# Performance work log

Hardware: AMD Instinct MI355X
Metric: run time of the kernel (lower is better)

Reference implementation:

```python
import jax, jax.numpy as jnp
import numpy as np

N, D, E, T, R, KMEM, DE = 50000, 128, 800000, 400000, 1, 32, 16
EPS = 1e-5
BETA_MAX = 5.0
GRAD_CLIP = 1.0
STATE_CLIP = 10.0
STEP = 0.1
DAMP = 0.9999  # update_damping=1.0 clamped to 1-1e-4 as in __init__


def segment_logsumexp(s, idx, n):
    # numerically-stable per-segment logsumexp; empty segments contribute 0
    m = jax.ops.segment_max(s, idx, num_segments=n)
    ms = jnp.where(jnp.isfinite(m), m, 0.0)
    z = jax.ops.segment_sum(jnp.exp(s - ms[idx]), idx, num_segments=n)
    return jnp.where(z > 0, jnp.log(jnp.maximum(z, 1e-30)) + ms, 0.0)


def setup_inputs() -> dict:
    key = jax.random.key(0)
    ks = jax.random.split(key, 24)
    inv1 = jnp.log(jnp.expm1(jnp.float32(1.0)))  # _inv_softplus(1.0)
    xav = 0.5 * np.sqrt(2.0 / (2 * D))  # xavier_uniform gain=0.5 ~ std
    inp = {
        'X': jax.random.normal(ks[0], (N, D), jnp.float32),
        'edge_attr': jax.random.normal(ks[1], (E, DE), jnp.float32),
        'ln_gamma': jnp.ones((D,), jnp.float32),
        'ln_beta': jnp.zeros((D,), jnp.float32),
        'W_Q2': jax.random.normal(ks[2], (D, D), jnp.float32) * xav,
        'W_K2': jax.random.normal(ks[3], (D, D), jnp.float32) * xav,
        'W_Q3': jax.random.normal(ks[4], (D, R * D), jnp.float32) * xav,
        'W_K3': jax.random.normal(ks[5], (D, R * D), jnp.float32) * xav,
        'T_tau': jax.random.normal(ks[6], (2, R, D), jnp.float32) * 0.02,
        'W_Qm': jax.random.normal(ks[7], (D, D), jnp.float32) * xav,
        'W_Km': jax.random.normal(ks[8], (D, D), jnp.float32) * xav,
        'B_mem': jax.random.normal(ks[9], (KMEM, D), jnp.float32) / np.sqrt(D),
        'We1': jax.random.normal(ks[10], (DE, D), jnp.float32) / np.sqrt(DE),
        'be1': jnp.zeros((D,), jnp.float32),
        'We2': jax.random.normal(ks[11], (D, 1), jnp.float32) / np.sqrt(D),
        'be2': jnp.zeros((1,), jnp.float32),
        'lambda_2': inv1, 'lambda_3': inv1, 'lambda_m': inv1,
        'beta_2': inv1, 'beta_3': inv1, 'beta_m': inv1,
        'c_2': jax.random.randint(ks[12], (E,), 0, N),
        'u_2': jax.random.randint(ks[13], (E,), 0, N),
        'c_3': jax.random.randint(ks[14], (T,), 0, N),
        'u_3': jax.random.randint(ks[15], (T,), 0, N),
        'v_3': jax.random.randint(ks[16], (T,), 0, N),
        't_tau': jax.random.randint(ks[17], (T,), 0, 2),
    }
    return inp


def reference(X, edge_attr, ln_gamma, ln_beta, W_Q2, W_K2, W_Q3, W_K3, T_tau,
              W_Qm, W_Km, B_mem, We1, be1, We2, be2,
              lambda_2, lambda_3, lambda_m, beta_2, beta_3, beta_m,
              c_2, u_2, c_3, u_3, v_3, t_tau):
    sqrt_d = jnp.sqrt(jnp.float32(D))

    def energy(Xv):
        mu = jnp.mean(Xv, axis=-1, keepdims=True)
        var = jnp.var(Xv, axis=-1, keepdims=True)
        G = (Xv - mu) * jax.lax.rsqrt(var + EPS) * ln_gamma + ln_beta
        # pairwise (order-2) energy over edge list
        b2 = jnp.minimum(jax.nn.softplus(beta_2), BETA_MAX)
        Q2, K2 = G @ W_Q2, G @ W_K2
        a2 = (jax.nn.gelu(edge_attr @ We1 + be1) @ We2 + be2)[:, 0]  # edge_mlp bias
        s2 = b2 * (jnp.sum(Q2[c_2] * K2[u_2], axis=-1) / sqrt_d) + a2  # [E]
        E2 = -(jax.nn.softplus(lambda_2) / b2) * jnp.sum(segment_logsumexp(s2, c_2, N))
        # triplet (order-3) energy with per-type tensor T_tau
        b3 = jnp.minimum(jax.nn.softplus(beta_3), BETA_MAX)
        Q3 = (G @ W_Q3).reshape(-1, R, D)
        K3 = (G @ W_K3).reshape(-1, R, D)
        s3 = b3 * jnp.einsum('erd,erd,erd,erd->e', Q3[c_3], K3[u_3], K3[v_3],
                             T_tau[t_tau]) / jnp.float32(D)  # [T]
        E3 = -(jax.nn.softplus(lambda_3) / b3) * jnp.sum(segment_logsumexp(s3, c_3, N))
        # memory-bank energy
        bm = jnp.minimum(jax.nn.softplus(beta_m), BETA_MAX)
        sm = bm * ((G @ W_Qm) @ (B_mem @ W_Km).T) / sqrt_d  # [N,K]
        Em = -(jax.nn.softplus(lambda_m) / bm) * jnp.sum(jax.nn.logsumexp(sm, axis=1))
        return E2 + E3 + Em

    Eval, gX = jax.value_and_grad(energy)(X)
    gn = jnp.maximum(jnp.linalg.norm(gX, axis=-1, keepdims=True), 1e-6)
    gX = gX * jnp.minimum(GRAD_CLIP / gn, 1.0)
    X_next = X - STEP * DAMP * gX
    sn = jnp.maximum(jnp.linalg.norm(X_next, axis=-1, keepdims=True), 1e-6)
    X_next = X_next * jnp.minimum(STATE_CLIP / sn, 1.0)
    return (X_next, Eval)
```

## Files before the change

### kernel.cpp

```cpp
#include <hip/hip_runtime.h>

#define NN 50000
#define DD 128
#define EE 800000
#define TT 400000
#define KM 32
#define UU 320
#define SCAN_TILE 2048
#define SCAN_NB ((NN + SCAN_TILE - 1) / SCAN_TILE)

static constexpr float INV_SQRT_D = 0.08838834764831845f;
static constexpr float INV_D = 1.f / 128.f;

typedef __attribute__((ext_vector_type(8))) short bf16x8;
typedef __attribute__((ext_vector_type(4))) float f32x4;
typedef unsigned short ushort_t;

__device__ __forceinline__ float softplus_f(float x) {
  return (x > 20.f) ? x : log1pf(__expf(x));
}

__device__ __forceinline__ float gelu_tanh(float x) {
  float x3 = x * x * x;
  float u = 0.7978845608028654f * (x + 0.044715f * x3);
  u = fminf(fmaxf(u, -15.f), 15.f);
  float e = __expf(2.f * u);
  float t = (e - 1.f) / (e + 1.f);
  return 0.5f * x * (1.f + t);
}

__device__ __forceinline__ float wredsum(float v) {
#pragma unroll
  for (int m = 32; m; m >>= 1) v += __shfl_xor(v, m, 64);
  return v;
}

__device__ __forceinline__ float redsum16(float v) {
#pragma unroll
  for (int m = 1; m < 16; m <<= 1) v += __shfl_xor(v, m, 64);
  return v;
}

__device__ __forceinline__ float blo(unsigned w) { return __uint_as_float(w << 16); }
__device__ __forceinline__ float bhi(unsigned w) { return __uint_as_float(w & 0xffff0000u); }
__device__ __forceinline__ unsigned pack_bf16(float a, float b) {
  unsigned ua = __float_as_uint(a); ua += 0x7fff + ((ua >> 16) & 1);
  unsigned ub = __float_as_uint(b); ub += 0x7fff + ((ub >> 16) & 1);
  return (ua >> 16) | (ub & 0xffff0000u);
}
__device__ __forceinline__ ushort_t bf16_1(float x) {
  unsigned u = __float_as_uint(x); u += 0x7fff + ((u >> 16) & 1);
  return (ushort_t)(u >> 16);
}
__device__ __forceinline__ void unp8(uint4 w, float* f) {
  f[0] = blo(w.x); f[1] = bhi(w.x); f[2] = blo(w.y); f[3] = bhi(w.y);
  f[4] = blo(w.z); f[5] = bhi(w.z); f[6] = blo(w.w); f[7] = bhi(w.w);
}
__device__ __forceinline__ uint4 pk8(const float* f) {
  uint4 r;
  r.x = pack_bf16(f[0], f[1]); r.y = pack_bf16(f[2], f[3]);
  r.z = pack_bf16(f[4], f[5]); r.w = pack_bf16(f[6], f[7]);
  return r;
}

__global__ void params_k(const float* l2, const float* l3, const float* lm,
                         const float* b2, const float* b3, const float* bm,
                         float* __restrict__ P) {
  if (threadIdx.x != 0) return;
  float B2 = fminf(softplus_f(b2[0]), 5.f);
  float B3 = fminf(softplus_f(b3[0]), 5.f);
  float Bm = fminf(softplus_f(bm[0]), 5.f);
  float S2 = softplus_f(l2[0]);
  float S3 = softplus_f(l3[0]);
  float Sm = softplus_f(lm[0]);
  P[0] = B2; P[1] = B3; P[2] = Bm;
  P[3] = -S2 * INV_SQRT_D; P[4] = -S3 * INV_D; P[5] = -Sm * INV_SQRT_D;
  P[6] = -S2 / B2; P[7] = -S3 / B3; P[8] = -Sm / Bm;
}

__global__ __launch_bounds__(256) void ln_fwd(const float* __restrict__ X,
                                              const float* __restrict__ gamma,
                                              const float* __restrict__ beta,
                                              unsigned* __restrict__ Gb,
                                              float* __restrict__ meanv,
                                              float* __restrict__ rstdv) {
  int row = blockIdx.x * 4 + (threadIdx.x >> 6);
  if (row >= NN) return;
  int l = threadIdx.x & 63;
  float2 x2 = *(const float2*)(X + row * DD + 2 * l);
  float mu = wredsum(x2.x + x2.y) * (1.f / DD);
  float d0 = x2.x - mu, d1 = x2.y - mu;
  float var = wredsum(d0 * d0 + d1 * d1) * (1.f / DD);
  float rstd = rsqrtf(var + 1e-5f);
  float2 g2 = *(const float2*)(gamma + 2 * l);
  float2 b2 = *(const float2*)(beta + 2 * l);
  float o0 = d0 * rstd * g2.x + b2.x;
  float o1 = d1 * rstd * g2.y + b2.y;
  Gb[(size_t)row * 64 + l] = pack_bf16(o0, o1);
  if (l == 0) { meanv[row] = mu; rstdv[row] = rstd; }
}

__global__ __launch_bounds__(256) void w_conv(const float* W0, const float* W1, const float* W2,
                                              const float* W3, const float* W4,
                                              ushort_t* __restrict__ Wt,
                                              ushort_t* __restrict__ Wc) {
  int idx = blockIdx.x * 256 + threadIdx.x;
  if (idx >= 640 * 128) return;
  const float* Ws[5] = {W0, W1, W2, W3, W4};
  int n = idx >> 7, k = idx & 127;
  Wt[idx] = bf16_1(Ws[n >> 7][(size_t)k * 128 + (n & 127)]);
  int k2 = idx >> 7, n2 = idx & 127;
  Wc[(size_t)n2 * 640 + k2] = bf16_1(Ws[k2 >> 7][(size_t)n2 * 128 + (k2 & 127)]);
}

__global__ __launch_bounds__(256) void mfma_fwd(const ushort_t* __restrict__ Gb,
                                                const ushort_t* __restrict__ Wt,
                                                ushort_t* __restrict__ QK, int M) {
  __shared__ ushort_t sB[64][136];
  int tid = threadIdx.x;
  int nb = blockIdx.y * 64;
  for (int idx = tid; idx < 64 * 16; idx += 256) {
    int r = idx >> 4, c8 = idx & 15;
    *(bf16x8*)&sB[r][c8 * 8] = *(const bf16x8*)(Wt + (size_t)(nb + r) * 128 + c8 * 8);
  }
  __syncthreads();
  int w = tid >> 6, l = tid & 63, quad = l >> 4, j = l & 15;
  int row0 = blockIdx.x * 64 + w * 16;
  int arow = row0 + j; if (arow >= M) arow = M - 1;
  const bf16x8* ap = (const bf16x8*)(Gb + (size_t)arow * 128);
  f32x4 acc[4];
#pragma unroll
  for (int nt = 0; nt < 4; nt++) acc[nt] = (f32x4){0.f, 0.f, 0.f, 0.f};
#pragma unroll
  for (int kc = 0; kc < 4; kc++) {
    bf16x8 a = ap[kc * 4 + quad];
#pragma unroll
    for (int nt = 0; nt < 4; nt++) {
      bf16x8 b = *(const bf16x8*)&sB[nt * 16 + j][kc * 32 + quad * 8];
      acc[nt] = __builtin_amdgcn_mfma_f32_16x16x32_bf16(a, b, acc[nt], 0, 0, 0);
    }
  }
#pragma unroll
  for (int nt = 0; nt < 4; nt++)
#pragma unroll
    for (int r = 0; r < 4; r++) {
      int row = row0 + quad * 4 + r;
      if (row < M) QK[(size_t)row * 640 + nb + nt * 16 + j] = bf16_1(acc[nt][r]);
    }
}

__global__ __launch_bounds__(256) void mfma_bwd(const ushort_t* __restrict__ dAll,
                                                const ushort_t* __restrict__ Wc,
                                                unsigned* __restrict__ dG, int M) {
  __shared__ ushort_t sB[64][40];
  int tid = threadIdx.x;
  int nb = blockIdx.y * 64;
  int w = tid >> 6, l = tid & 63, quad = l >> 4, j = l & 15;
  int row0 = blockIdx.x * 64 + w * 16;
  int arow = row0 + j; if (arow >= M) arow = M - 1;
  const ushort_t* arp = dAll + (size_t)arow * 640;
  f32x4 acc[4];
#pragma unroll
  for (int nt = 0; nt < 4; nt++) acc[nt] = (f32x4){0.f, 0.f, 0.f, 0.f};
  int sr = tid >> 2, sc = tid & 3;
  for (int kc = 0; kc < 20; kc++) {
    __syncthreads();
    *(bf16x8*)&sB[sr][sc * 8] = *(const bf16x8*)(Wc + (size_t)(nb + sr) * 640 + kc * 32 + sc * 8);
    __syncthreads();
    bf16x8 a = *(const bf16x8*)(arp + kc * 32 + quad * 8);
#pragma unroll
    for (int nt = 0; nt < 4; nt++) {
      bf16x8 b = *(const bf16x8*)&sB[nt * 16 + j][quad * 8];
      acc[nt] = __builtin_amdgcn_mfma_f32_16x16x32_bf16(a, b, acc[nt], 0, 0, 0);
    }
  }
#pragma unroll
  for (int nt = 0; nt < 4; nt++)
#pragma unroll
    for (int r = 0; r < 4; r++) {
      int row = row0 + quad * 4 + r;
      if (row < M) ((ushort_t*)dG)[(size_t)row * 128 + nb + nt * 16 + j] = bf16_1(acc[nt][r]);
    }
}

__global__ __launch_bounds__(256, 1) void gemm_km(const float* __restrict__ A,
                                                  const float* __restrict__ W,
                                                  float* __restrict__ C, int M) {
  __shared__ float As[32][132];
  __shared__ float Wst[128][136];
  const int tid = threadIdx.x;
  for (int idx = tid; idx < 128 * 128; idx += 256) {
    int k = idx >> 7, jj = idx & 127;
    Wst[k][jj] = W[k * 128 + jj];
  }
  for (int idx = tid; idx < 32 * 128; idx += 256) {
    int r = idx >> 7, d = idx & 127;
    As[r][d] = A[r * 128 + d];
  }
  __syncthreads();
  int r = tid >> 3, c0 = (tid & 7) * 16;
  float acc[16];
#pragma unroll
  for (int q = 0; q < 16; q++) acc[q] = 0.f;
  for (int k = 0; k < 128; k++) {
    float av = As[r][k];
#pragma unroll
    for (int q = 0; q < 16; q++) acc[q] = fmaf(av, Wst[k][c0 + q], acc[q]);
  }
#pragma unroll
  for (int q = 0; q < 16; q++) C[r * 128 + c0 + q] = acc[q];
}

__global__ __launch_bounds__(256) void edge_mlp(const float* __restrict__ EA,
                                                const float* __restrict__ We1,
                                                const float* __restrict__ be1,
                                                const float* __restrict__ We2,
                                                const float* __restrict__ be2,
                                                float* __restrict__ a2) {
  __shared__ float sW1[16 * 128];
  __shared__ float sb1[128];
  __shared__ float sW2[128];
  int tid = threadIdx.x;
  for (int i = tid; i < 2048; i += 256) sW1[i] = We1[i];
  if (tid < 128) { sb1[tid] = be1[tid]; sW2[tid] = We2[tid]; }
  __syncthreads();
  int w = tid >> 6, l = tid & 63;
  int m = l & 15, q = l >> 4;
  union u8 { bf16x8 v; ushort_t s[8]; };
  u8 bf[8];
  float bb[8], ww[8];
#pragma unroll
  for (int nt = 0; nt < 8; nt++) {
    int n = nt * 16 + m;
#pragma unroll
    for (int j = 0; j < 8; j++) {
      int k = q * 8 + j;
      bf[nt].s[j] = (k < 16) ? bf16_1(sW1[k * 128 + n]) : (ushort_t)0;
    }
    bb[nt] = sb1[n];
    ww[nt] = sW2[n];
  }
  float be2v = be2[0];
  for (int batch = 0; batch < 4; batch++) {
    int e0 = blockIdx.x * 256 + batch * 64 + w * 16;
    u8 af;
    if (q < 2) {
      const float* ep = EA + (size_t)(e0 + m) * 16 + q * 8;
      float4 v0 = *(const float4*)ep;
      float4 v1 = *(const float4*)(ep + 4);
      af.s[0] = bf16_1(v0.x); af.s[1] = bf16_1(v0.y);
      af.s[2] = bf16_1(v0.z); af.s[3] = bf16_1(v0.w);
      af.s[4] = bf16_1(v1.x); af.s[5] = bf16_1(v1.y);
      af.s[6] = bf16_1(v1.z); af.s[7] = bf16_1(v1.w);
    } else {
#pragma unroll
      for (int j = 0; j < 8; j++) af.s[j] = 0;
    }
    f32x4 z4 = (f32x4){0.f, 0.f, 0.f, 0.f};
    float s0 = 0.f, s1 = 0.f, s2 = 0.f, s3 = 0.f;
#pragma unroll
    for (int nt = 0; nt < 8; nt++) {
      f32x4 acc = __builtin_amdgcn_mfma_f32_16x16x32_bf16(af.v, bf[nt].v, z4, 0, 0, 0);
      float bias = bb[nt], w2v = ww[nt];
      s0 = fmaf(gelu_tanh(acc[0] + bias), w2v, s0);
      s1 = fmaf(gelu_tanh(acc[1] + bias), w2v, s1);
      s2 = fmaf(gelu_tanh(acc[2] + bias), w2v, s2);
      s3 = fmaf(gelu_tanh(acc[3] + bias), w2v, s3);
    }
    s0 = redsum16(s0); s1 = redsum16(s1); s2 = redsum16(s2); s3 = redsum16(s3);
    if (m == 0) {
      int eb = e0 + q * 4;
      a2[eb + 0] = s0 + be2v;
      a2[eb + 1] = s1 + be2v;
      a2[eb + 2] = s2 + be2v;
      a2[eb + 3] = s3 + be2v;
    }
  }
}

__global__ __launch_bounds__(256) void hist2(const int* __restrict__ a,
                                             const int* __restrict__ b,
                                             int* __restrict__ ca,
                                             int* __restrict__ cb, int n) {
  int e = blockIdx.x * 256 + threadIdx.x;
  if (e >= n) return;
  atomicAdd(&ca[a[e]], 1);
  atomicAdd(&cb[b[e]], 1);
}

__global__ __launch_bounds__(256) void hist_t3(const int* __restrict__ c,
                                               const int* __restrict__ u,
                                               const int* __restrict__ v,
                                               int* __restrict__ cc,
                                               int* __restrict__ cuv, int n) {
  int t = blockIdx.x * 256 + threadIdx.x;
  if (t >= n) return;
  atomicAdd(&cc[c[t]], 1);
  atomicAdd(&cuv[u[t]], 1);
  atomicAdd(&cuv[v[t]], 1);
}

__global__ __launch_bounds__(256) void scan_p1(const int* __restrict__ cnt,
                                               int* __restrict__ part) {
  int arr = blockIdx.y, b = blockIdx.x;
  const int* c = cnt + (size_t)arr * NN;
  int gi = b * SCAN_TILE + threadIdx.x * 8;
  int s = 0;
#pragma unroll
  for (int t = 0; t < 8; t++) s += (gi + t < NN) ? c[gi + t] : 0;
#pragma unroll
  for (int m = 32; m; m >>= 1) s += __shfl_xor(s, m, 64);
  __shared__ int wt[4];
  int lane = threadIdx.x & 63, wid = threadIdx.x >> 6;
  if (lane == 0) wt[wid] = s;
  __syncthreads();
  if (threadIdx.x == 0) part[arr * SCAN_NB + b] = wt[0] + wt[1] + wt[2] + wt[3];
}

__global__ __launch_bounds__(256) void scan_p2(int* __restrict__ part) {
  int w = threadIdx.x >> 6, l = threadIdx.x & 63;
  int v = (l < SCAN_NB) ? part[w * SCAN_NB + l] : 0;
  int x = v;
#pragma unroll
  for (int d = 1; d < 64; d <<= 1) {
    int y = __shfl_up(x, d, 64);
    if (l >= d) x += y;
  }
  if (l < SCAN_NB) part[w * SCAN_NB + l] = x - v;
}

__global__ __launch_bounds__(256) void scan_p3(const int* __restrict__ cnt,
                                               const int* __restrict__ part,
                                               int* __restrict__ rowptr,
                                               int* __restrict__ cursor) {
  int arr = blockIdx.y, b = blockIdx.x;
  const int* c = cnt + (size_t)arr * NN;
  int* rp = rowptr + (size_t)arr * (NN + 1);
  int* cur = cursor + (size_t)arr * NN;
  int tid = threadIdx.x;
  int gi = b * SCAN_TILE + tid * 8;
  int vals[8];
#pragma unroll
  for (int t = 0; t < 8; t++) vals[t] = (gi + t < NN) ? c[gi + t] : 0;
  int tsum = 0;
#pragma unroll
  for (int t = 0; t < 8; t++) tsum += vals[t];
  int lane = tid & 63, wid = tid >> 6;
  int x = tsum;
#pragma unroll
  for (int d = 1; d < 64; d <<= 1) {
    int y = __shfl_up(x, d, 64);
    if (lane >= d) x += y;
  }
  __shared__ int wt[4];
  if (lane == 63) wt[wid] = x;
  __syncthreads();
  int wadd = 0;
  for (int w = 0; w < wid; w++) wadd += wt[w];
  int running = part[arr * SCAN_NB + b] + wadd + x - tsum;
#pragma unroll
  for (int t = 0; t < 8; t++) {
    if (gi + t < NN) { rp[gi + t] = running; cur[gi + t] = running; }
    running += vals[t];
  }
  if (b == SCAN_NB - 1 && tid == 255) rp[NN] = running;
}

__global__ __launch_bounds__(256) void scat2(const int* __restrict__ c2,
                                             const int* __restrict__ u2,
                                             const float* __restrict__ a2,
                                             int* __restrict__ cuc,
                                             int* __restrict__ cuu,
                                             int* __restrict__ part_c,
                                             float* __restrict__ apay_c,
                                             int* __restrict__ slot_u,
                                             int* __restrict__ part_u, int n) {
  int e = blockIdx.x * 256 + threadIdx.x;
  if (e >= n) return;
  int c = c2[e], u = u2[e];
  int p = atomicAdd(&cuc[c], 1);
  part_c[p] = u; apay_c[p] = a2[e];
  int p2 = atomicAdd(&cuu[u], 1);
  slot_u[p2] = p; part_u[p2] = c;
}

__global__ __launch_bounds__(256) void scat_t3(const int* __restrict__ c3,
                                               const int* __restrict__ u3,
                                               const int* __restrict__ v3,
                                               const int* __restrict__ ttau,
                                               int* __restrict__ cuc,
                                               int* __restrict__ cuv,
                                               int* __restrict__ pu_c,
                                               int* __restrict__ pv_c,
                                               int* __restrict__ ta_c,
                                               int* __restrict__ po,
                                               int* __restrict__ pc,
                                               int* __restrict__ spk, int n) {
  int t = blockIdx.x * 256 + threadIdx.x;
  if (t >= n) return;
  int c = c3[t], u = u3[t], v = v3[t], ta = ttau[t] & 1;
  int p = atomicAdd(&cuc[c], 1);
  pu_c[p] = u; pv_c[p] = v; ta_c[p] = ta;
  int sp = (p << 1) | ta;
  int q1 = atomicAdd(&cuv[u], 1);
  po[q1] = v; pc[q1] = c; spk[q1] = sp;
  int q2 = atomicAdd(&cuv[v], 1);
  po[q2] = u; pc[q2] = c; spk[q2] = sp;
}

__global__ __launch_bounds__(256) void e2_fused(const unsigned* __restrict__ QK,
                                                const float* __restrict__ P,
                                                const int* __restrict__ part,
                                                const float* __restrict__ apay,
                                                const int* __restrict__ rp,
                                                float* __restrict__ s2c,
                                                float* __restrict__ L2,
                                                unsigned* __restrict__ dAll) {
  int row = blockIdx.x * 4 + (threadIdx.x >> 6);
  if (row >= NN) return;
  int l = threadIdx.x & 63, g = l >> 4, j = l & 15;
  float b2s = P[0] * INV_SQRT_D, cw2 = P[3];
  float q[8];
  unp8(*(const uint4*)(QK + (size_t)row * UU + j * 4), q);
  int s = rp[row], e = rp[row + 1];
  float m = -3.0e38f, z = 0.f;
  float acc[8] = {0.f, 0.f, 0.f, 0.f, 0.f, 0.f, 0.f, 0.f};
  int i0 = s + g;
  uint4 kA = {0, 0, 0, 0}, kB = {0, 0, 0, 0};
  float aA = 0.f, aB = 0.f;
  if (i0 < e) {
    int u = part[i0]; aA = apay[i0];
    kA = *(const uint4*)(QK + (size_t)u * UU + 64 + j * 4);
  }
  if (i0 + 4 < e) {
    int u = part[i0 + 4]; aB = apay[i0 + 4];
    kB = *(const uint4*)(QK + (size_t)u * UU + 64 + j * 4);
  }
  for (int i = i0; i < e; i += 4) {
    uint4 kC = {0, 0, 0, 0}; float aC = 0.f;
    if (i + 8 < e) {
      int u = part[i + 8]; aC = apay[i + 8];
      kC = *(const uint4*)(QK + (size_t)u * UU + 64 + j * 4);
    }
    float k[8]; unp8(kA, k);
    float d = 0.f;
#pragma unroll
    for (int t = 0; t < 8; t++) d = fmaf(q[t], k[t], d);
    d = redsum16(d);
    float sv = b2s * d + aA;
    if (j == 0) s2c[i] = sv;
    if (sv <= m) {
      float p = __expf(sv - m);
      z += p;
#pragma unroll
      for (int t = 0; t < 8; t++) acc[t] = fmaf(p, k[t], acc[t]);
    } else {
      float r = __expf(m - sv);
      z = fmaf(z, r, 1.f);
#pragma unroll
      for (int t = 0; t < 8; t++) acc[t] = fmaf(acc[t], r, k[t]);
      m = sv;
    }
    kA = kB; aA = aB; kB = kC; aB = aC;
  }
  float mx = fmaxf(m, __shfl_xor(m, 16, 64));
  mx = fmaxf(mx, __shfl_xor(mx, 32, 64));
  float r = (z > 0.f) ? __expf(m - mx) : 0.f;
  float zz = z * r;
  zz += __shfl_xor(zz, 16, 64);
  zz += __shfl_xor(zz, 32, 64);
#pragma unroll
  for (int t = 0; t < 8; t++) {
    float v = acc[t] * r;
    v += __shfl_xor(v, 16, 64);
    v += __shfl_xor(v, 32, 64);
    acc[t] = v;
  }
  if (l == 0) L2[row] = (zz > 0.f) ? (mx + __logf(zz)) : 0.f;
  if (g == 0) {
    float coef = (zz > 0.f) ? cw2 / zz : 0.f;
    float o[8];
#pragma unroll
    for (int t = 0; t < 8; t++) o[t] = coef * acc[t];
    *(uint4*)(dAll + (size_t)row * UU + 0 + j * 4) = pk8(o);
  }
}

__global__ __launch_bounds__(256) void dk2_gather(const unsigned* __restrict__ QK,
                                                  const float* __restrict__ s2c,
                                                  const float* __restrict__ L2,
                                                  const float* __restrict__ P,
                                                  const int* __restrict__ slot,
                                                  const int* __restrict__ part,
                                                  const int* __restrict__ rp,
                                                  unsigned* __restrict__ dAll) {
  int row = blockIdx.x * 4 + (threadIdx.x >> 6);
  if (row >= NN) return;
  int l = threadIdx.x & 63, g = l >> 4, j = l & 15;
  float cw2 = P[3];
  int s = rp[row], e = rp[row + 1];
  float acc[8] = {0.f, 0.f, 0.f, 0.f, 0.f, 0.f, 0.f, 0.f};
  int i0 = s + g;
  uint4 qA = {0, 0, 0, 0}, qB = {0, 0, 0, 0};
  float scA = 0.f, lcA = 0.f, scB = 0.f, lcB = 0.f;
  if (i0 < e) {
    int c = part[i0]; scA = s2c[slot[i0]]; lcA = L2[c];
    qA = *(const uint4*)(QK + (size_t)c * UU + 0 + j * 4);
  }
  if (i0 + 4 < e) {
    int c = part[i0 + 4]; scB = s2c[slot[i0 + 4]]; lcB = L2[c];
    qB = *(const uint4*)(QK + (size_t)c * UU + 0 + j * 4);
  }
  for (int i = i0; i < e; i += 4) {
    uint4 qC = {0, 0, 0, 0}; float scC = 0.f, lcC = 0.f;
    if (i + 8 < e) {
      int c = part[i + 8]; scC = s2c[slot[i + 8]]; lcC = L2[c];
      qC = *(const uint4*)(QK + (size_t)c * UU + 0 + j * 4);
    }
    float w = cw2 * __expf(scA - lcA);
    float qv[8]; unp8(qA, qv);
#pragma unroll
    for (int t = 0; t < 8; t++) acc[t] = fmaf(w, qv[t], acc[t]);
    qA = qB; scA = scB; lcA = lcB;
    qB = qC; scB = scC; lcB = lcC;
  }
#pragma unroll
  for (int t = 0; t < 8; t++) {
    float v = acc[t];
    v += __shfl_xor(v, 16, 64);
    v += __shfl_xor(v, 32, 64);
    acc[t] = v;
  }
  if (g == 0) *(uint4*)(dAll + (size_t)row * UU + 64 + j * 4) = pk8(acc);
}

__global__ __launch_bounds__(256) void t3_fused(const unsigned* __restrict__ QK,
                                                const float* __restrict__ Tt,
                                                const float* __restrict__ P,
                                                const int* __restrict__ pu,
                                                const int* __restrict__ pv,
                                                const int* __restrict__ tac,
                                                const int* __restrict__ rp,
                                                float* __restrict__ s3c,
                                                float* __restrict__ L3,
                                                unsigned* __restrict__ dAll) {
  __shared__ float sT[2 * DD];
  int tid = threadIdx.x;
  sT[tid] = Tt[tid];
  __syncthreads();
  int row = blockIdx.x * 4 + (tid >> 6);
  if (row >= NN) return;
  int l = tid & 63, g = l >> 4, j = l & 15;
  float b3s = P[1] * INV_D, cw3 = P[4];
  float q[8];
  unp8(*(const uint4*)(QK + (size_t)row * UU + 128 + j * 4), q);
  int s = rp[row], e = rp[row + 1];
  float m = -3.0e38f, z = 0.f;
  float acc[8] = {0.f, 0.f, 0.f, 0.f, 0.f, 0.f, 0.f, 0.f};
  int i0 = s + g;
  uint4 kuA = {0, 0, 0, 0}, kvA = {0, 0, 0, 0};
  uint4 kuB = {0, 0, 0, 0}, kvB = {0, 0, 0, 0};
  int taA = 0, taB = 0;
  if (i0 < e) {
    int u = pu[i0], v = pv[i0]; taA = tac[i0];
    kuA = *(const uint4*)(QK + (size_t)u * UU + 192 + j * 4);
    kvA = *(const uint4*)(QK + (size_t)v * UU + 192 + j * 4);
  }
  if (i0 + 4 < e) {
    int u = pu[i0 + 4], v = pv[i0 + 4]; taB = tac[i0 + 4];
    kuB = *(const uint4*)(QK + (size_t)u * UU + 192 + j * 4);
    kvB = *(const uint4*)(QK + (size_t)v * UU + 192 + j * 4);
  }
  for (int i = i0; i < e; i += 4) {
    uint4 kuC = {0, 0, 0, 0}, kvC = {0, 0, 0, 0}; int taC = 0;
    if (i + 8 < e) {
      int u = pu[i + 8], v = pv[i + 8]; taC = tac[i + 8];
      kuC = *(const uint4*)(QK + (size_t)u * UU + 192 + j * 4);
      kvC = *(const uint4*)(QK + (size_t)v * UU + 192 + j * 4);
    }
    float ku[8], kv[8]; unp8(kuA, ku); unp8(kvA, kv);
    const float* tv = &sT[taA * DD + j * 8];
    float et[8], d = 0.f;
#pragma unroll
    for (int t = 0; t < 8; t++) { et[t] = ku[t] * kv[t] * tv[t]; d = fmaf(q[t], et[t], d); }
    d = redsum16(d);
    float sv = b3s * d;
    if (j == 0) s3c[i] = sv;
    if (sv <= m) {
      float p = __expf(sv - m);
      z += p;
#pragma unroll
      for (int t = 0; t < 8; t++) acc[t] = fmaf(p, et[t], acc[t]);
    } else {
      float r = __expf(m - sv);
      z = fmaf(z, r, 1.f);
#pragma unroll
      for (int t = 0; t < 8; t++) acc[t] = fmaf(acc[t], r, et[t]);
      m = sv;
    }
    kuA = kuB; kvA = kvB; taA = taB;
    kuB = kuC; kvB = kvC; taB = taC;
  }
  float mx = fmaxf(m, __shfl_xor(m, 16, 64));
  mx = fmaxf(mx, __shfl_xor(mx, 32, 64));
  float r = (z > 0.f) ? __expf(m - mx) : 0.f;
  float zz = z * r;
  zz += __shfl_xor(zz, 16, 64);
  zz += __shfl_xor(zz, 32, 64);
#pragma unroll
  for (int t = 0; t < 8; t++) {
    float v = acc[t] * r;
    v += __shfl_xor(v, 16, 64);
    v += __shfl_xor(v, 32, 64);
    acc[t] = v;
  }
  if (l == 0) L3[row] = (zz > 0.f) ? (mx + __logf(zz)) : 0.f;
  if (g == 0) {
    float coef = (zz > 0.f) ? cw3 / zz : 0.f;
    float o[8];
#pragma unroll
    for (int t = 0; t < 8; t++) o[t] = coef * acc[t];
    *(uint4*)(dAll + (size_t)row * UU + 128 + j * 4) = pk8(o);
  }
}

__global__ __launch_bounds__(256) void dk3_gather(const unsigned* __restrict__ QK,
                                                  const float* __restrict__ Tt,
                                                  const float* __restrict__ s3c,
                                                  const float* __restrict__ L3,
                                                  const float* __restrict__ P,
                                                  const int* __restrict__ po,
                                                  const int* __restrict__ pc,
                                                  const int* __restrict__ spk,
                                                  const int* __restrict__ rp,
                                                  unsigned* __restrict__ dAll) {
  __shared__ float sT[2 * DD];
  int tid = threadIdx.x;
  sT[tid] = Tt[tid];
  __syncthreads();
  int row = blockIdx.x * 4 + (tid >> 6);
  if (row >= NN) return;
  int l = tid & 63, g = l >> 4, j = l & 15;
  float cw3 = P[4];
  int s = rp[row], e = rp[row + 1];
  float acc[8] = {0.f, 0.f, 0.f, 0.f, 0.f, 0.f, 0.f, 0.f};
  int i0 = s + g;
  uint4 qA = {0, 0, 0, 0}, kA = {0, 0, 0, 0};
  uint4 qB = {0, 0, 0, 0}, kB = {0, 0, 0, 0};
  int taA = 0, taB = 0;
  float scA = 0.f, lcA = 0.f, scB = 0.f, lcB = 0.f;
  if (i0 < e) {
    int o = po[i0], c = pc[i0], sp = spk[i0];
    taA = sp & 1; scA = s3c[sp >> 1]; lcA = L3[c];
    qA = *(const uint4*)(QK + (size_t)c * UU + 128 + j * 4);
    kA = *(const uint4*)(QK + (size_t)o * UU + 192 + j * 4);
  }
  if (i0 + 4 < e) {
    int o = po[i0 + 4], c = pc[i0 + 4], sp = spk[i0 + 4];
    taB = sp & 1; scB = s3c[sp >> 1]; lcB = L3[c];
    qB = *(const uint4*)(QK + (size_t)c * UU + 128 + j * 4);
    kB = *(const uint4*)(QK + (size_t)o * UU + 192 + j * 4);
  }
  for (int i = i0; i < e; i += 4) {
    uint4 qC = {0, 0, 0, 0}, kC = {0, 0, 0, 0}; int taC = 0;
    float scC = 0.f, lcC = 0.f;
    if (i + 8 < e) {
      int o = po[i + 8], c = pc[i + 8], sp = spk[i + 8];
      taC = sp & 1; scC = s3c[sp >> 1]; lcC = L3[c];
      qC = *(const uint4*)(QK + (size_t)c * UU + 128 + j * 4);
      kC = *(const uint4*)(QK + (size_t)o * UU + 192 + j * 4);
    }
    float w = cw3 * __expf(scA - lcA);
    float qv[8], ko[8]; unp8(qA, qv); unp8(kA, ko);
    const float* tv = &sT[taA * DD + j * 8];
#pragma unroll
    for (int t = 0; t < 8; t++) acc[t] = fmaf(w * tv[t], qv[t] * ko[t], acc[t]);
    qA = qB; kA = kB; taA = taB; scA = scB; lcA = lcB;
    qB = qC; kB = kC; taB = taC; scB = scC; lcB = lcC;
  }
#pragma unroll
  for (int t = 0; t < 8; t++) {
    float v = acc[t];
    v += __shfl_xor(v, 16, 64);
    v += __shfl_xor(v, 32, 64);
    acc[t] = v;
  }
  if (g == 0) *(uint4*)(dAll + (size_t)row * UU + 192 + j * 4) = pk8(acc);
}

__global__ __launch_bounds__(256) void em_row(const unsigned* __restrict__ QK,
                                              const float* __restrict__ Km,
                                              const float* __restrict__ P,
                                              unsigned* __restrict__ dAll,
                                              float* __restrict__ Lm) {
  __shared__ float sKm[KM * DD];
  int tid = threadIdx.x;
  for (int i = tid; i < KM * DD; i += 256) sKm[i] = Km[i];
  __syncthreads();
  int row = blockIdx.x * 4 + (tid >> 6);
  if (row >= NN) return;
  int l = tid & 63, g = l >> 4, j = l & 15;
  float bms = P[2] * INV_SQRT_D, cwm = P[5];
  float q[8];
  unp8(*(const uint4*)(QK + (size_t)row * UU + 256 + j * 4), q);
  float dk[8];
#pragma unroll
  for (int kk = 0; kk < 8; kk++) {
    int k = g * 8 + kk;
    const float* kr = &sKm[k * DD + j * 8];
    float d = 0.f;
#pragma unroll
    for (int t = 0; t < 8; t++) d = fmaf(q[t], kr[t], d);
    dk[kk] = redsum16(d) * bms;
  }
  float m = dk[0];
#pragma unroll
  for (int kk = 1; kk < 8; kk++) m = fmaxf(m, dk[kk]);
  float mx = fmaxf(m, __shfl_xor(m, 16, 64));
  mx = fmaxf(mx, __shfl_xor(mx, 32, 64));
  float p[8], z = 0.f;
#pragma unroll
  for (int kk = 0; kk < 8; kk++) { p[kk] = __expf(dk[kk] - mx); z += p[kk]; }
  float zz = z;
  zz += __shfl_xor(zz, 16, 64);
  zz += __shfl_xor(zz, 32, 64);
  if (l == 0) Lm[row] = mx + __logf(zz);
  float coef = cwm / zz;
  float acc[8] = {0.f, 0.f, 0.f, 0.f, 0.f, 0.f, 0.f, 0.f};
#pragma unroll
  for (int kk = 0; kk < 8; kk++) {
    int k = g * 8 + kk;
    const float* kr = &sKm[k * DD + j * 8];
    float pc_ = p[kk] * coef;
#pragma unroll
    for (int t = 0; t < 8; t++) acc[t] = fmaf(pc_, kr[t], acc[t]);
  }
#pragma unroll
  for (int t = 0; t < 8; t++) {
    float v = acc[t];
    v += __shfl_xor(v, 16, 64);
    v += __shfl_xor(v, 32, 64);
    acc[t] = v;
  }
  if (g == 0) *(uint4*)(dAll + (size_t)row * UU + 256 + j * 4) = pk8(acc);
}

__global__ __launch_bounds__(256) void ln_bwd(const float* __restrict__ X,
                                              const unsigned* __restrict__ dG,
                                              const float* __restrict__ gamma,
                                              const float* __restrict__ meanv,
                                              const float* __restrict__ rstdv,
                                              float* __restrict__ out) {
  int row = blockIdx.x * 4 + (threadIdx.x >> 6);
  if (row >= NN) return;
  int l = threadIdx.x & 63;
  float mu = meanv[row], rstd = rstdv[row];
  float2 x2 = *(const float2*)(X + row * DD + 2 * l);
  unsigned gw = dG[(size_t)row * 64 + l];
  float2 ga = *(const float2*)(gamma + 2 * l);
  float xh0 = (x2.x - mu) * rstd, xh1 = (x2.y - mu) * rstd;
  float dh0 = blo(gw) * ga.x, dh1 = bhi(gw) * ga.y;
  float sa = wredsum(dh0 + dh1) * (1.f / DD);
  float sb = wredsum(dh0 * xh0 + dh1 * xh1) * (1.f / DD);
  float dx0 = rstd * (dh0 - sa - xh0 * sb);
  float dx1 = rstd * (dh1 - sa - xh1 * sb);
  float gn = fmaxf(sqrtf(wredsum(dx0 * dx0 + dx1 * dx1)), 1e-6f);
  float sc = fminf(1.f / gn, 1.f);
  dx0 *= sc; dx1 *= sc;
  float xn0 = x2.x - 0.1f * 0.9999f * dx0;
  float xn1 = x2.y - 0.1f * 0.9999f * dx1;
  float sn = fmaxf(sqrtf(wredsum(xn0 * xn0 + xn1 * xn1)), 1e-6f);
  float sc2 = fminf(10.f / sn, 1.f);
  float2 o; o.x = xn0 * sc2; o.y = xn1 * sc2;
  *(float2*)(out + row * DD + 2 * l) = o;
}

__global__ __launch_bounds__(256) void eval_write(const float* __restrict__ L2,
                                                  const float* __restrict__ L3,
                                                  const float* __restrict__ Lm,
                                                  const float* __restrict__ P,
                                                  float* __restrict__ out) {
  int i = blockIdx.x * 256 + threadIdx.x;
  float a2 = 0.f, a3 = 0.f, am = 0.f;
  if (i < NN) { a2 = L2[i]; a3 = L3[i]; am = Lm[i]; }
  a2 = wredsum(a2); a3 = wredsum(a3); am = wredsum(am);
  __shared__ float r2[4], r3[4], rm[4];
  int wv = threadIdx.x >> 6, l = threadIdx.x & 63;
  if (l == 0) { r2[wv] = a2; r3[wv] = a3; rm[wv] = am; }
  __syncthreads();
  if (threadIdx.x == 0) {
    float S2 = r2[0] + r2[1] + r2[2] + r2[3];
    float S3 = r3[0] + r3[1] + r3[2] + r3[3];
    float Sm = rm[0] + rm[1] + rm[2] + rm[3];
    atomicAdd(out, P[6] * S2 + P[7] * S3 + P[8] * Sm);
  }
}

extern "C" void kernel_launch(void* const* d_in, const int* in_sizes, int n_in,
                              void* d_out, int out_size, void* d_ws, size_t ws_size,
                              hipStream_t stream) {
  (void)in_sizes; (void)n_in; (void)out_size;
  const float* X = (const float*)d_in[0];
  const float* EA = (const float*)d_in[1];
  const float* ln_g = (const float*)d_in[2];
  const float* ln_b = (const float*)d_in[3];
  const float* W_Q2 = (const float*)d_in[4];
  const float* W_K2 = (const float*)d_in[5];
  const float* W_Q3 = (const float*)d_in[6];
  const float* W_K3 = (const float*)d_in[7];
  const float* T_tau = (const float*)d_in[8];
  const float* W_Qm = (const float*)d_in[9];
  const float* W_Km = (const float*)d_in[10];
  const float* B_mem = (const float*)d_in[11];
  const float* We1 = (const float*)d_in[12];
  const float* be1 = (const float*)d_in[13];
  const float* We2 = (const float*)d_in[14];
  const float* be2 = (const float*)d_in[15];
  const float* l2s = (const float*)d_in[16];
  const float* l3s = (const float*)d_in[17];
  const float* lms = (const float*)d_in[18];
  const float* b2s = (const float*)d_in[19];
  const float* b3s = (const float*)d_in[20];
  const float* bms = (const float*)d_in[21];
  const int* c2 = (const int*)d_in[22];
  const int* u2 = (const int*)d_in[23];
  const int* c3 = (const int*)d_in[24];
  const int* u3 = (const int*)d_in[25];
  const int* v3 = (const int*)d_in[26];
  const int* ttau = (const int*)d_in[27];
  float* out = (float*)d_out;

  float* ws = (float*)d_ws;
  size_t off = 0;
  auto alloc = [&](size_t n) { float* p = ws + off; off += n; return p; };
  const size_t ND = (size_t)NN * DD;
  unsigned* Gb = (unsigned*)alloc(ND / 2);
  unsigned* QKall = (unsigned*)alloc((size_t)NN * UU);
  unsigned* dAll = (unsigned*)alloc((size_t)NN * UU);
  unsigned* dG = (unsigned*)alloc(ND / 2);
  ushort_t* Wt5 = (ushort_t*)alloc(640 * 128 / 2);
  ushort_t* Wcat = (ushort_t*)alloc(640 * 128 / 2);
  float* Km = alloc((size_t)KM * DD);
  float* a2 = alloc(EE);
  float* s2c = alloc(EE);
  float* s3c = alloc(TT);
  float* meanv = alloc(NN);
  float* rstdv = alloc(NN);
  float* L2 = alloc(NN);
  float* L3 = alloc(NN);
  float* Lm = alloc(NN);
  float* Pparams = alloc(16);
  int* cnt = (int*)alloc(4 * (size_t)NN);
  int* rowptr = (int*)alloc(4 * (size_t)(NN + 1));
  int* cursor = (int*)alloc(4 * (size_t)NN);
  int* spart = (int*)alloc(4 * SCAN_NB);
  int* part_c2 = (int*)alloc(EE);
  float* apay_c2 = alloc(EE);
  int* slot_u2 = (int*)alloc(EE);
  int* part_u2 = (int*)alloc(EE);
  int* pu_c3 = (int*)alloc(TT);
  int* pv_c3 = (int*)alloc(TT);
  int* ta_c3 = (int*)alloc(TT);
  int* po_uv = (int*)alloc(2 * (size_t)TT);
  int* pc_uv = (int*)alloc(2 * (size_t)TT);
  int* spk_uv = (int*)alloc(2 * (size_t)TT);
  if (off * sizeof(float) > ws_size) return;

  int* cnt_c2 = cnt, *cnt_u2 = cnt + NN, *cnt_c3 = cnt + 2 * NN, *cnt_uv = cnt + 3 * NN;
  int* rp_c2 = rowptr, *rp_u2 = rowptr + (NN + 1), *rp_c3 = rowptr + 2 * (NN + 1), *rp_uv = rowptr + 3 * (NN + 1);
  int* cu_c2 = cursor, *cu_u2 = cursor + NN, *cu_c3 = cursor + 2 * NN, *cu_uv = cursor + 3 * NN;

  hipMemsetAsync(cnt, 0, 4ull * NN * sizeof(int), stream);
  hipMemsetAsync(out + ND, 0, sizeof(float), stream);

  params_k<<<1, 64, 0, stream>>>(l2s, l3s, lms, b2s, b3s, bms, Pparams);

  int rowB = (NN + 3) / 4;
  int mB = (NN + 63) / 64;

  ln_fwd<<<rowB, 256, 0, stream>>>(X, ln_g, ln_b, Gb, meanv, rstdv);
  w_conv<<<320, 256, 0, stream>>>(W_Q2, W_K2, W_Q3, W_K3, W_Qm, Wt5, Wcat);
  mfma_fwd<<<dim3(mB, 10), 256, 0, stream>>>((const ushort_t*)Gb, Wt5, (ushort_t*)QKall, NN);
  gemm_km<<<1, 256, 0, stream>>>(B_mem, W_Km, Km, KM);
  edge_mlp<<<EE / 256, 256, 0, stream>>>(EA, We1, be1, We2, be2, a2);

  hist2<<<(EE + 255) / 256, 256, 0, stream>>>(c2, u2, cnt_c2, cnt_u2, EE);
  hist_t3<<<(TT + 255) / 256, 256, 0, stream>>>(c3, u3, v3, cnt_c3, cnt_uv, TT);
  scan_p1<<<dim3(SCAN_NB, 4), 256, 0, stream>>>(cnt, spart);
  scan_p2<<<1, 256, 0, stream>>>(spart);
  scan_p3<<<dim3(SCAN_NB, 4), 256, 0, stream>>>(cnt, spart, rowptr, cursor);
  scat2<<<(EE + 255) / 256, 256, 0, stream>>>(c2, u2, a2, cu_c2, cu_u2,
                                              part_c2, apay_c2, slot_u2, part_u2, EE);
  scat_t3<<<(TT + 255) / 256, 256, 0, stream>>>(c3, u3, v3, ttau, cu_c3, cu_uv,
                                                pu_c3, pv_c3, ta_c3,
                                                po_uv, pc_uv, spk_uv, TT);

  e2_fused<<<rowB, 256, 0, stream>>>(QKall, Pparams, part_c2, apay_c2, rp_c2, s2c, L2, dAll);
  dk2_gather<<<rowB, 256, 0, stream>>>(QKall, s2c, L2, Pparams, slot_u2, part_u2, rp_u2, dAll);
  t3_fused<<<rowB, 256, 0, stream>>>(QKall, T_tau, Pparams, pu_c3, pv_c3, ta_c3, rp_c3, s3c, L3, dAll);
  dk3_gather<<<rowB, 256, 0, stream>>>(QKall, T_tau, s3c, L3, Pparams, po_uv, pc_uv, spk_uv, rp_uv, dAll);
  em_row<<<rowB, 256, 0, stream>>>(QKall, Km, Pparams, dAll, Lm);

  mfma_bwd<<<dim3(mB, 2), 256, 0, stream>>>((const ushort_t*)dAll, Wcat, dG, NN);

  ln_bwd<<<rowB, 256, 0, stream>>>(X, dG, ln_g, meanv, rstdv, out);
  eval_write<<<(NN + 255) / 256, 256, 0, stream>>>(L2, L3, Lm, Pparams, out + ND);
}
```

Measured before the change: 900.8 us.

## Pack CSR edge payloads into uint2 records and cheapen the edge-MLP GELU

The separate per-edge CSR arrays (partner, payload, slot, type) become interleaved uint2 records, with node pairs packed as 16-bit fields for the triplet lists. Each gather kernel then issues one 8-byte load per neighbour instead of two or three scattered 4-byte loads, and the scatter kernels write fewer streams. The edge MLP folds the bias into the MFMA accumulator input and replaces tanh-GELU with a sigmoid form using a hardware reciprocal. The 16-bit packing relies on N=50000 fitting in 16 bits, and the GELU rewrite changes rounding slightly.

```diff
diff --git a/kernel.cpp b/kernel.cpp
--- a/kernel.cpp
+++ b/kernel.cpp
@@ -20,13 +20,10 @@
   return (x > 20.f) ? x : log1pf(__expf(x));
 }
 
-__device__ __forceinline__ float gelu_tanh(float x) {
-  float x3 = x * x * x;
-  float u = 0.7978845608028654f * (x + 0.044715f * x3);
-  u = fminf(fmaxf(u, -15.f), 15.f);
-  float e = __expf(2.f * u);
-  float t = (e - 1.f) / (e + 1.f);
-  return 0.5f * x * (1.f + t);
+__device__ __forceinline__ float gelu_fast(float x) {
+  float p = fmaf(0.044715f * x * x, x, x);
+  float e = __expf(-1.5957691216057308f * p);
+  return x * __builtin_amdgcn_rcpf(1.f + e);
 }
 
 __device__ __forceinline__ float wredsum(float v) {
@@ -256,16 +253,17 @@
 #pragma unroll
       for (int j = 0; j < 8; j++) af.s[j] = 0;
     }
-    f32x4 z4 = (f32x4){0.f, 0.f, 0.f, 0.f};
     float s0 = 0.f, s1 = 0.f, s2 = 0.f, s3 = 0.f;
 #pragma unroll
     for (int nt = 0; nt < 8; nt++) {
-      f32x4 acc = __builtin_amdgcn_mfma_f32_16x16x32_bf16(af.v, bf[nt].v, z4, 0, 0, 0);
-      float bias = bb[nt], w2v = ww[nt];
-      s0 = fmaf(gelu_tanh(acc[0] + bias), w2v, s0);
-      s1 = fmaf(gelu_tanh(acc[1] + bias), w2v, s1);
-      s2 = fmaf(gelu_tanh(acc[2] + bias), w2v, s2);
-      s3 = fmaf(gelu_tanh(acc[3] + bias), w2v, s3);
+      float bias = bb[nt];
+      f32x4 cin = (f32x4){bias, bias, bias, bias};
+      f32x4 acc = __builtin_amdgcn_mfma_f32_16x16x32_bf16(af.v, bf[nt].v, cin, 0, 0, 0);
+      float w2v = ww[nt];
+      s0 = fmaf(gelu_fast(acc[0]), w2v, s0);
+      s1 = fmaf(gelu_fast(acc[1]), w2v, s1);
+      s2 = fmaf(gelu_fast(acc[2]), w2v, s2);
+      s3 = fmaf(gelu_fast(acc[3]), w2v, s3);
     }
     s0 = redsum16(s0); s1 = redsum16(s1); s2 = redsum16(s2); s3 = redsum16(s3);
     if (m == 0) {
@@ -371,17 +369,17 @@
                                              const float* __restrict__ a2,
                                              int* __restrict__ cuc,
                                              int* __restrict__ cuu,
-                                             int* __restrict__ part_c,
-                                             float* __restrict__ apay_c,
-                                             int* __restrict__ slot_u,
-                                             int* __restrict__ part_u, int n) {
+                                             uint2* __restrict__ payc,
+                                             uint2* __restrict__ payu, int n) {
   int e = blockIdx.x * 256 + threadIdx.x;
   if (e >= n) return;
   int c = c2[e], u = u2[e];
   int p = atomicAdd(&cuc[c], 1);
-  part_c[p] = u; apay_c[p] = a2[e];
   int p2 = atomicAdd(&cuu[u], 1);
-  slot_u[p2] = p; part_u[p2] = c;
+  uint2 t; t.x = (unsigned)u; t.y = __float_as_uint(a2[e]);
+  payc[p] = t;
+  uint2 t2; t2.x = (unsigned)p; t2.y = (unsigned)c;
+  payu[p2] = t2;
 }
 
 __global__ __launch_bounds__(256) void scat_t3(const int* __restrict__ c3,
@@ -390,28 +388,26 @@
                                                const int* __restrict__ ttau,
                                                int* __restrict__ cuc,
                                                int* __restrict__ cuv,
-                                               int* __restrict__ pu_c,
-                                               int* __restrict__ pv_c,
-                                               int* __restrict__ ta_c,
-                                               int* __restrict__ po,
-                                               int* __restrict__ pc,
-                                               int* __restrict__ spk, int n) {
+                                               uint2* __restrict__ payc,
+                                               uint2* __restrict__ payuv, int n) {
   int t = blockIdx.x * 256 + threadIdx.x;
   if (t >= n) return;
   int c = c3[t], u = u3[t], v = v3[t], ta = ttau[t] & 1;
   int p = atomicAdd(&cuc[c], 1);
-  pu_c[p] = u; pv_c[p] = v; ta_c[p] = ta;
-  int sp = (p << 1) | ta;
   int q1 = atomicAdd(&cuv[u], 1);
-  po[q1] = v; pc[q1] = c; spk[q1] = sp;
   int q2 = atomicAdd(&cuv[v], 1);
-  po[q2] = u; pc[q2] = c; spk[q2] = sp;
+  unsigned sp = ((unsigned)p << 1) | (unsigned)ta;
+  uint2 a; a.x = ((unsigned)u << 16) | (unsigned)v; a.y = (unsigned)ta;
+  payc[p] = a;
+  uint2 b1; b1.x = ((unsigned)v << 16) | (unsigned)c; b1.y = sp;
+  payuv[q1] = b1;
+  uint2 b2; b2.x = ((unsigned)u << 16) | (unsigned)c; b2.y = sp;
+  payuv[q2] = b2;
 }
 
 __global__ __launch_bounds__(256) void e2_fused(const unsigned* __restrict__ QK,
                                                 const float* __restrict__ P,
-                                                const int* __restrict__ part,
-                                                const float* __restrict__ apay,
+                                                const uint2* __restrict__ pay,
                                                 const int* __restrict__ rp,
                                                 float* __restrict__ s2c,
                                                 float* __restrict__ L2,
@@ -429,18 +425,18 @@
   uint4 kA = {0, 0, 0, 0}, kB = {0, 0, 0, 0};
   float aA = 0.f, aB = 0.f;
   if (i0 < e) {
-    int u = part[i0]; aA = apay[i0];
-    kA = *(const uint4*)(QK + (size_t)u * UU + 64 + j * 4);
+    uint2 w = pay[i0]; aA = __uint_as_float(w.y);
+    kA = *(const uint4*)(QK + (size_t)w.x * UU + 64 + j * 4);
   }
   if (i0 + 4 < e) {
-    int u = part[i0 + 4]; aB = apay[i0 + 4];
-    kB = *(const uint4*)(QK + (size_t)u * UU + 64 + j * 4);
+    uint2 w = pay[i0 + 4]; aB = __uint_as_float(w.y);
+    kB = *(const uint4*)(QK + (size_t)w.x * UU + 64 + j * 4);
   }
   for (int i = i0; i < e; i += 4) {
     uint4 kC = {0, 0, 0, 0}; float aC = 0.f;
     if (i + 8 < e) {
-      int u = part[i + 8]; aC = apay[i + 8];
-      kC = *(const uint4*)(QK + (size_t)u * UU + 64 + j * 4);
+      uint2 w = pay[i + 8]; aC = __uint_as_float(w.y);
+      kC = *(const uint4*)(QK + (size_t)w.x * UU + 64 + j * 4);
     }
     float k[8]; unp8(kA, k);
     float d = 0.f;
@@ -490,8 +486,7 @@
                                                   const float* __restrict__ s2c,
                                                   const float* __restrict__ L2,
                                                   const float* __restrict__ P,
-                                                  const int* __restrict__ slot,
-                                                  const int* __restrict__ part,
+                                                  const uint2* __restrict__ pay,
                                                   const int* __restrict__ rp,
                                                   unsigned* __restrict__ dAll) {
   int row = blockIdx.x * 4 + (threadIdx.x >> 6);
@@ -504,18 +499,18 @@
   uint4 qA = {0, 0, 0, 0}, qB = {0, 0, 0, 0};
   float scA = 0.f, lcA = 0.f, scB = 0.f, lcB = 0.f;
   if (i0 < e) {
-    int c = part[i0]; scA = s2c[slot[i0]]; lcA = L2[c];
-    qA = *(const uint4*)(QK + (size_t)c * UU + 0 + j * 4);
+    uint2 w = pay[i0]; scA = s2c[w.x]; lcA = L2[w.y];
+    qA = *(const uint4*)(QK + (size_t)w.y * UU + 0 + j * 4);
   }
   if (i0 + 4 < e) {
-    int c = part[i0 + 4]; scB = s2c[slot[i0 + 4]]; lcB = L2[c];
-    qB = *(const uint4*)(QK + (size_t)c * UU + 0 + j * 4);
+    uint2 w = pay[i0 + 4]; scB = s2c[w.x]; lcB = L2[w.y];
+    qB = *(const uint4*)(QK + (size_t)w.y * UU + 0 + j * 4);
   }
   for (int i = i0; i < e; i += 4) {
     uint4 qC = {0, 0, 0, 0}; float scC = 0.f, lcC = 0.f;
     if (i + 8 < e) {
-      int c = part[i + 8]; scC = s2c[slot[i + 8]]; lcC = L2[c];
-      qC = *(const uint4*)(QK + (size_t)c * UU + 0 + j * 4);
+      uint2 w = pay[i + 8]; scC = s2c[w.x]; lcC = L2[w.y];
+      qC = *(const uint4*)(QK + (size_t)w.y * UU + 0 + j * 4);
     }
     float w = cw2 * __expf(scA - lcA);
     float qv[8]; unp8(qA, qv);
@@ -537,9 +532,7 @@
 __global__ __launch_bounds__(256) void t3_fused(const unsigned* __restrict__ QK,
                                                 const float* __restrict__ Tt,
                                                 const float* __restrict__ P,
-                                                const int* __restrict__ pu,
-                                                const int* __restrict__ pv,
-                                                const int* __restrict__ tac,
+                                                const uint2* __restrict__ pay,
                                                 const int* __restrict__ rp,
                                                 float* __restrict__ s3c,
                                                 float* __restrict__ L3,
@@ -562,19 +555,19 @@
   uint4 kuB = {0, 0, 0, 0}, kvB = {0, 0, 0, 0};
   int taA = 0, taB = 0;
   if (i0 < e) {
-    int u = pu[i0], v = pv[i0]; taA = tac[i0];
+    uint2 w = pay[i0]; int u = w.x >> 16, v = w.x & 0xffff; taA = (int)w.y;
     kuA = *(const uint4*)(QK + (size_t)u * UU + 192 + j * 4);
     kvA = *(const uint4*)(QK + (size_t)v * UU + 192 + j * 4);
   }
   if (i0 + 4 < e) {
-    int u = pu[i0 + 4], v = pv[i0 + 4]; taB = tac[i0 + 4];
+    uint2 w = pay[i0 + 4]; int u = w.x >> 16, v = w.x & 0xffff; taB = (int)w.y;
     kuB = *(const uint4*)(QK + (size_t)u * UU + 192 + j * 4);
     kvB = *(const uint4*)(QK + (size_t)v * UU + 192 + j * 4);
   }
   for (int i = i0; i < e; i += 4) {
     uint4 kuC = {0, 0, 0, 0}, kvC = {0, 0, 0, 0}; int taC = 0;
     if (i + 8 < e) {
-      int u = pu[i + 8], v = pv[i + 8]; taC = tac[i + 8];
+      uint2 w = pay[i + 8]; int u = w.x >> 16, v = w.x & 0xffff; taC = (int)w.y;
       kuC = *(const uint4*)(QK + (size_t)u * UU + 192 + j * 4);
       kvC = *(const uint4*)(QK + (size_t)v * UU + 192 + j * 4);
     }
@@ -629,9 +622,7 @@
                                                   const float* __restrict__ s3c,
                                                   const float* __restrict__ L3,
                                                   const float* __restrict__ P,
-                                                  const int* __restrict__ po,
-                                                  const int* __restrict__ pc,
-                                                  const int* __restrict__ spk,
+                                                  const uint2* __restrict__ pay,
                                                   const int* __restrict__ rp,
                                                   unsigned* __restrict__ dAll) {
   __shared__ float sT[2 * DD];
@@ -650,14 +641,14 @@
   int taA = 0, taB = 0;
   float scA = 0.f, lcA = 0.f, scB = 0.f, lcB = 0.f;
   if (i0 < e) {
-    int o = po[i0], c = pc[i0], sp = spk[i0];
-    taA = sp & 1; scA = s3c[sp >> 1]; lcA = L3[c];
+    uint2 w = pay[i0]; int o = w.x >> 16, c = w.x & 0xffff; unsigned sp = w.y;
+    taA = (int)(sp & 1); scA = s3c[sp >> 1]; lcA = L3[c];
     qA = *(const uint4*)(QK + (size_t)c * UU + 128 + j * 4);
     kA = *(const uint4*)(QK + (size_t)o * UU + 192 + j * 4);
   }
   if (i0 + 4 < e) {
-    int o = po[i0 + 4], c = pc[i0 + 4], sp = spk[i0 + 4];
-    taB = sp & 1; scB = s3c[sp >> 1]; lcB = L3[c];
+    uint2 w = pay[i0 + 4]; int o = w.x >> 16, c = w.x & 0xffff; unsigned sp = w.y;
+    taB = (int)(sp & 1); scB = s3c[sp >> 1]; lcB = L3[c];
     qB = *(const uint4*)(QK + (size_t)c * UU + 128 + j * 4);
     kB = *(const uint4*)(QK + (size_t)o * UU + 192 + j * 4);
   }
@@ -665,8 +656,8 @@
     uint4 qC = {0, 0, 0, 0}, kC = {0, 0, 0, 0}; int taC = 0;
     float scC = 0.f, lcC = 0.f;
     if (i + 8 < e) {
-      int o = po[i + 8], c = pc[i + 8], sp = spk[i + 8];
-      taC = sp & 1; scC = s3c[sp >> 1]; lcC = L3[c];
+      uint2 w = pay[i + 8]; int o = w.x >> 16, c = w.x & 0xffff; unsigned sp = w.y;
+      taC = (int)(sp & 1); scC = s3c[sp >> 1]; lcC = L3[c];
       qC = *(const uint4*)(QK + (size_t)c * UU + 128 + j * 4);
       kC = *(const uint4*)(QK + (size_t)o * UU + 192 + j * 4);
     }
@@ -854,16 +845,10 @@
   int* rowptr = (int*)alloc(4 * (size_t)(NN + 1));
   int* cursor = (int*)alloc(4 * (size_t)NN);
   int* spart = (int*)alloc(4 * SCAN_NB);
-  int* part_c2 = (int*)alloc(EE);
-  float* apay_c2 = alloc(EE);
-  int* slot_u2 = (int*)alloc(EE);
-  int* part_u2 = (int*)alloc(EE);
-  int* pu_c3 = (int*)alloc(TT);
-  int* pv_c3 = (int*)alloc(TT);
-  int* ta_c3 = (int*)alloc(TT);
-  int* po_uv = (int*)alloc(2 * (size_t)TT);
-  int* pc_uv = (int*)alloc(2 * (size_t)TT);
-  int* spk_uv = (int*)alloc(2 * (size_t)TT);
+  uint2* payc2 = (uint2*)alloc(2 * (size_t)EE);
+  uint2* payu2 = (uint2*)alloc(2 * (size_t)EE);
+  uint2* payc3 = (uint2*)alloc(2 * (size_t)TT);
+  uint2* payuv = (uint2*)alloc(4 * (size_t)TT);
   if (off * sizeof(float) > ws_size) return;
 
   int* cnt_c2 = cnt, *cnt_u2 = cnt + NN, *cnt_c3 = cnt + 2 * NN, *cnt_uv = cnt + 3 * NN;
@@ -889,16 +874,14 @@
   scan_p1<<<dim3(SCAN_NB, 4), 256, 0, stream>>>(cnt, spart);
   scan_p2<<<1, 256, 0, stream>>>(spart);
   scan_p3<<<dim3(SCAN_NB, 4), 256, 0, stream>>>(cnt, spart, rowptr, cursor);
-  scat2<<<(EE + 255) / 256, 256, 0, stream>>>(c2, u2, a2, cu_c2, cu_u2,
-                                              part_c2, apay_c2, slot_u2, part_u2, EE);
+  scat2<<<(EE + 255) / 256, 256, 0, stream>>>(c2, u2, a2, cu_c2, cu_u2, payc2, payu2, EE);
   scat_t3<<<(TT + 255) / 256, 256, 0, stream>>>(c3, u3, v3, ttau, cu_c3, cu_uv,
-                                                pu_c3, pv_c3, ta_c3,
-                                                po_uv, pc_uv, spk_uv, TT);
-
-  e2_fused<<<rowB, 256, 0, stream>>>(QKall, Pparams, part_c2, apay_c2, rp_c2, s2c, L2, dAll);
-  dk2_gather<<<rowB, 256, 0, stream>>>(QKall, s2c, L2, Pparams, slot_u2, part_u2, rp_u2, dAll);
-  t3_fused<<<rowB, 256, 0, stream>>>(QKall, T_tau, Pparams, pu_c3, pv_c3, ta_c3, rp_c3, s3c, L3, dAll);
-  dk3_gather<<<rowB, 256, 0, stream>>>(QKall, T_tau, s3c, L3, Pparams, po_uv, pc_uv, spk_uv, rp_uv, dAll);
+                                                payc3, payuv, TT);
+
+  e2_fused<<<rowB, 256, 0, stream>>>(QKall, Pparams, payc2, rp_c2, s2c, L2, dAll);
+  dk2_gather<<<rowB, 256, 0, stream>>>(QKall, s2c, L2, Pparams, payu2, rp_u2, dAll);
+  t3_fused<<<rowB, 256, 0, stream>>>(QKall, T_tau, Pparams, payc3, rp_c3, s3c, L3, dAll);
+  dk3_gather<<<rowB, 256, 0, stream>>>(QKall, T_tau, s3c, L3, Pparams, payuv, rp_uv, dAll);
   em_row<<<rowB, 256, 0, stream>>>(QKall, Km, Pparams, dAll, Lm);
 
   mfma_bwd<<<dim3(mB, 2), 256, 0, stream>>>((const ushort_t*)dAll, Wcat, dG, NN);
```

New measurement: 930.8 us. +3.3%, slower.
